# Performance work log

Hardware: AMD Instinct MI355X
Metric: run time of the kernel (lower is better)

The kernel has to match this reference:

```python
import math
import jax, jax.numpy as jnp
import numpy as np

GROUPS = 32
EPS = 1e-5


def group_norm(x, w, b):
    # x: [B, C, H, W]
    B, C, H, W = x.shape
    xg = x.reshape(B, GROUPS, C // GROUPS, H, W)
    mean = xg.mean(axis=(2, 3, 4), keepdims=True)
    var = xg.var(axis=(2, 3, 4), keepdims=True)
    xg = (xg - mean) * jax.lax.rsqrt(var + EPS)
    x = xg.reshape(B, C, H, W)
    return x * w[None, :, None, None] + b[None, :, None, None]


def setup_inputs() -> dict:
    key = jax.random.key(0)
    ks = jax.random.split(key, 4)
    B, C, H, W = 16, 512, 32, 32
    x = jax.random.normal(ks[0], (B, C, H, W), dtype=jnp.float32)
    norm_w = jnp.ones((C,), dtype=jnp.float32)
    norm_b = jnp.zeros((C,), dtype=jnp.float32)
    qkv_w = jax.random.normal(ks[1], (3 * C, C), dtype=jnp.float32) / math.sqrt(C)
    qkv_b = jnp.zeros((3 * C,), dtype=jnp.float32)
    proj_w = jax.random.normal(ks[2], (C, C), dtype=jnp.float32) / math.sqrt(C)
    proj_b = jnp.zeros((C,), dtype=jnp.float32)
    return {"x": x, "norm_w": norm_w, "norm_b": norm_b,
            "qkv_w": qkv_w, "qkv_b": qkv_b,
            "proj_w": proj_w, "proj_b": proj_b}


def reference(x, norm_w, norm_b, qkv_w, qkv_b, proj_w, proj_b):
    B, C, H, W = x.shape
    xn = group_norm(x, norm_w, norm_b)
    # 1x1 conv == channel matmul: [B,3C,H,W]
    qkv = jnp.einsum('oc,bchw->bohw', qkv_w, xn) + qkv_b[None, :, None, None]
    q, k, v = jnp.split(qkv, 3, axis=1)
    q = q.reshape(B, C, H * W).transpose(0, 2, 1)  # [B, HW, C]
    k = k.reshape(B, C, H * W)                     # [B, C, HW]
    v = v.reshape(B, C, H * W).transpose(0, 2, 1)  # [B, HW, C]
    attn = jax.nn.softmax(jnp.einsum('bnc,bcm->bnm', q, k) / math.sqrt(C), axis=-1)
    h = jnp.einsum('bnm,bmc->bnc', attn, v)        # [B, HW, C]
    h = h.transpose(0, 2, 1).reshape(B, C, H, W)
    out = jnp.einsum('oc,bchw->bohw', proj_w, h) + proj_b[None, :, None, None]
    return out + x
```

## Files before the change

kernel.cpp:

```cpp
#include <hip/hip_runtime.h>

#define GLD16(gp, lp) __builtin_amdgcn_global_load_lds( \
    (const __attribute__((address_space(1))) void*)(gp), \
    (__attribute__((address_space(3))) void*)(lp), 16, 0, 0)

typedef __attribute__((ext_vector_type(8))) short bf16x8;
typedef __attribute__((ext_vector_type(4))) float f32x4;

__device__ __forceinline__ short f2bf(float f) {
    union { float f; unsigned u; } x; x.f = f;
    unsigned r = x.u + 0x7fffu + ((x.u >> 16) & 1u);
    return (short)(r >> 16);
}
__device__ __forceinline__ float bf2f(short s) {
    union { unsigned u; float f; } x;
    x.u = ((unsigned)(unsigned short)s) << 16;
    return x.f;
}
__device__ __forceinline__ int xcd_swz(int id, int n) {
    return (id & 7) * (n >> 3) + (id >> 3);
}

__global__ __launch_bounds__(256) void prep(
    const float* __restrict__ qkv_w, const float* __restrict__ proj_w,
    short* __restrict__ wq, short* __restrict__ wp,
    const float* __restrict__ x, float* __restrict__ mean, float* __restrict__ rstd)
{
    if (blockIdx.x < 1024) {
        int idx = blockIdx.x * 256 + threadIdx.x;
        const int NQ4 = (1536 * 512) / 4;
        float4 f; short4 s;
        if (idx < NQ4) {
            f = ((const float4*)qkv_w)[idx];
            s.x = f2bf(f.x); s.y = f2bf(f.y); s.z = f2bf(f.z); s.w = f2bf(f.w);
            ((short4*)wq)[idx] = s;
        } else {
            int j = idx - NQ4;
            f = ((const float4*)proj_w)[j];
            s.x = f2bf(f.x); s.y = f2bf(f.y); s.z = f2bf(f.z); s.w = f2bf(f.w);
            ((short4*)wp)[j] = s;
        }
    } else {
        int bg = blockIdx.x - 1024;
        const float4* p = (const float4*)(x + (size_t)bg * 16384);
        float s = 0.f, ss = 0.f;
        for (int i = threadIdx.x; i < 4096; i += 256) {
            float4 v = p[i];
            s  += v.x + v.y + v.z + v.w;
            ss += v.x * v.x + v.y * v.y + v.z * v.z + v.w * v.w;
        }
        #pragma unroll
        for (int o = 32; o > 0; o >>= 1) {
            s  += __shfl_down(s, o);
            ss += __shfl_down(ss, o);
        }
        __shared__ float ls[4], lss[4];
        int wave = threadIdx.x >> 6;
        if ((threadIdx.x & 63) == 0) { ls[wave] = s; lss[wave] = ss; }
        __syncthreads();
        if (threadIdx.x == 0) {
            s  = ls[0] + ls[1] + ls[2] + ls[3];
            ss = lss[0] + lss[1] + lss[2] + lss[3];
            float m = s * (1.f / 16384.f);
            float var = ss * (1.f / 16384.f) - m * m;
            mean[bg] = m;
            rstd[bg] = rsqrtf(var + 1e-5f);
        }
    }
}

__global__ __launch_bounds__(256) void gn_apply_t(
    const float* __restrict__ x, const float* __restrict__ w, const float* __restrict__ bb,
    const float* __restrict__ mean, const float* __restrict__ rstd,
    short* __restrict__ xnT)
{
    __shared__ short tile[64][65];
    int b = blockIdx.z, cblk = blockIdx.y, nblk = blockIdx.x;
    int t = threadIdx.x;
    int nl = t & 63;
    int cb = t >> 6;
    #pragma unroll
    for (int i = 0; i < 16; ++i) {
        int cl = cb * 16 + i;
        int cg = cblk * 64 + cl;
        int bgid = b * 32 + (cg >> 4);
        float sc = rstd[bgid] * w[cg];
        float sh = bb[cg] - mean[bgid] * sc;
        float xv = x[((size_t)(b * 512 + cg)) * 1024 + nblk * 64 + nl];
        tile[cl][nl] = f2bf(xv * sc + sh);
    }
    __syncthreads();
    int ng = t >> 4;
    int c4 = (t & 15) * 4;
    #pragma unroll
    for (int p = 0; p < 4; ++p) {
        int nl2 = p * 16 + ng;
        short4 sv;
        sv.x = tile[c4 + 0][nl2];
        sv.y = tile[c4 + 1][nl2];
        sv.z = tile[c4 + 2][nl2];
        sv.w = tile[c4 + 3][nl2];
        *(short4*)&xnT[((size_t)(b * 1024 + nblk * 64 + nl2)) * 512 + cblk * 64 + c4] = sv;
    }
}

template<int NT>
__device__ __forceinline__ void gemm256_8p(
    const short* __restrict__ A, const short* __restrict__ B,
    const int lda, const int ldb, short* lds, f32x4 acc[8][4])
{
    const int tid  = threadIdx.x;
    const int lane = tid & 63;
    const int wave = tid >> 6;
    const int wm = wave >> 2;
    const int wn = wave & 3;
    const int fr = lane & 15;
    const int fk = lane >> 4;

    const short* pa[2]; const short* pb[2]; int la[2], lb[2];
    #pragma unroll
    for (int i = 0; i < 2; ++i) {
        int cid = i * 512 + tid;
        int row = cid >> 2, sl = cid & 3;
        int csw = sl ^ ((row >> 1) & 3);
        pa[i] = A + (size_t)row * lda + csw * 8;
        pb[i] = B + (size_t)row * ldb + csw * 8;
        la[i] = cid * 8;
        lb[i] = 8192 + cid * 8;
    }

    #pragma unroll
    for (int i = 0; i < 2; ++i) GLD16(pa[i],      lds + la[i]);
    #pragma unroll
    for (int i = 0; i < 2; ++i) GLD16(pb[i],      lds + lb[i]);
    #pragma unroll
    for (int i = 0; i < 2; ++i) GLD16(pa[i] + 32, lds + 16384 + la[i]);
    #pragma unroll
    for (int i = 0; i < 2; ++i) GLD16(pb[i] + 32, lds + 16384 + lb[i]);
    asm volatile("s_waitcnt vmcnt(4)" ::: "memory");
    asm volatile("s_barrier" ::: "memory");

    const int arow0 = wm * 128 + fr;
    const int brow0 = wn * 64 + fr;

    int base = 0, sbase = 32768, kst = 64;
    for (int t = 0; t < NT; ++t) {
        const short* lA = lds + base;
        const short* lB = lds + base + 8192;
        const bool pre = (t + 2 < NT);

        if (pre) {
            GLD16(pa[0] + kst, lds + sbase + la[0]);
            GLD16(pa[1] + kst, lds + sbase + la[1]);
        }
        bf16x8 af[8], bf0[2];
        #pragma unroll
        for (int m = 0; m < 8; ++m) {
            int R = arow0 + m * 16;
            af[m] = *(const bf16x8*)&lA[R * 32 + ((fk ^ ((R >> 1) & 3)) << 3)];
        }
        #pragma unroll
        for (int n = 0; n < 2; ++n) {
            int R = brow0 + n * 16;
            bf0[n] = *(const bf16x8*)&lB[R * 32 + ((fk ^ ((R >> 1) & 3)) << 3)];
        }
        asm volatile("s_barrier" ::: "memory");
        __builtin_amdgcn_s_setprio(1);
        #pragma unroll
        for (int m = 0; m < 8; ++m)
            #pragma unroll
            for (int n = 0; n < 2; ++n)
                acc[m][n] = __builtin_amdgcn_mfma_f32_16x16x32_bf16(af[m], bf0[n], acc[m][n], 0, 0, 0);
        __builtin_amdgcn_s_setprio(0);

        if (pre) {
            GLD16(pb[0] + kst, lds + sbase + lb[0]);
            GLD16(pb[1] + kst, lds + sbase + lb[1]);
        }
        bf16x8 bf1[2];
        #pragma unroll
        for (int n = 0; n < 2; ++n) {
            int R = brow0 + (n + 2) * 16;
            bf1[n] = *(const bf16x8*)&lB[R * 32 + ((fk ^ ((R >> 1) & 3)) << 3)];
        }
        asm volatile("s_barrier" ::: "memory");
        __builtin_amdgcn_s_setprio(1);
        #pragma unroll
        for (int m = 0; m < 8; ++m)
            #pragma unroll
            for (int n = 0; n < 2; ++n)
                acc[m][n + 2] = __builtin_amdgcn_mfma_f32_16x16x32_bf16(af[m], bf1[n], acc[m][n + 2], 0, 0, 0);
        __builtin_amdgcn_s_setprio(0);

        if (pre)                 asm volatile("s_waitcnt vmcnt(4)" ::: "memory");
        else if (t + 1 < NT)     asm volatile("s_waitcnt vmcnt(0)" ::: "memory");
        asm volatile("s_barrier" ::: "memory");
        __builtin_amdgcn_sched_barrier(0);
        base  = (base  == 32768) ? 0 : base  + 16384;
        sbase = (sbase == 32768) ? 0 : sbase + 16384;
        kst += 32;
    }
}

template<int NT>
__device__ __forceinline__ void gemm128x256(
    const short* __restrict__ A, const short* __restrict__ B,
    const int lda, const int ldb, short* lds, f32x4 acc[4][4])
{
    const int tid  = threadIdx.x;
    const int lane = tid & 63;
    const int wave = tid >> 6;
    const int wm = wave >> 2;
    const int wn = wave & 3;
    const int fr = lane & 15;
    const int fk = lane >> 4;

    const short* pa; int la;
    {
        int row = tid >> 2, sl = tid & 3;
        int csw = sl ^ ((row >> 1) & 3);
        pa = A + (size_t)row * lda + csw * 8;
        la = tid * 8;
    }
    const short* pb[2]; int lb[2];
    #pragma unroll
    for (int i = 0; i < 2; ++i) {
        int cid = i * 512 + tid;
        int row = cid >> 2, sl = cid & 3;
        int csw = sl ^ ((row >> 1) & 3);
        pb[i] = B + (size_t)row * ldb + csw * 8;
        lb[i] = 4096 + cid * 8;
    }

    GLD16(pa, lds + la);
    #pragma unroll
    for (int i = 0; i < 2; ++i) GLD16(pb[i], lds + lb[i]);
    GLD16(pa + 32, lds + 12288 + la);
    #pragma unroll
    for (int i = 0; i < 2; ++i) GLD16(pb[i] + 32, lds + 12288 + lb[i]);
    asm volatile("s_waitcnt vmcnt(3)" ::: "memory");
    asm volatile("s_barrier" ::: "memory");

    const int arow0 = wm * 64 + fr;
    const int brow0 = wn * 64 + fr;

    int base = 0, sbase = 24576, kst = 64;
    for (int t = 0; t < NT; ++t) {
        const short* lA = lds + base;
        const short* lB = lds + base + 4096;
        const bool pre = (t + 2 < NT);

        if (pre) GLD16(pa + kst, lds + sbase + la);
        bf16x8 af[4], bf0[2];
        #pragma unroll
        for (int m = 0; m < 4; ++m) {
            int R = arow0 + m * 16;
            af[m] = *(const bf16x8*)&lA[R * 32 + ((fk ^ ((R >> 1) & 3)) << 3)];
        }
        #pragma unroll
        for (int n = 0; n < 2; ++n) {
            int R = brow0 + n * 16;
            bf0[n] = *(const bf16x8*)&lB[R * 32 + ((fk ^ ((R >> 1) & 3)) << 3)];
        }
        asm volatile("s_barrier" ::: "memory");
        __builtin_amdgcn_s_setprio(1);
        #pragma unroll
        for (int m = 0; m < 4; ++m)
            #pragma unroll
            for (int n = 0; n < 2; ++n)
                acc[m][n] = __builtin_amdgcn_mfma_f32_16x16x32_bf16(af[m], bf0[n], acc[m][n], 0, 0, 0);
        __builtin_amdgcn_s_setprio(0);

        if (pre) {
            GLD16(pb[0] + kst, lds + sbase + lb[0]);
            GLD16(pb[1] + kst, lds + sbase + lb[1]);
        }
        bf16x8 bf1[2];
        #pragma unroll
        for (int n = 0; n < 2; ++n) {
            int R = brow0 + (n + 2) * 16;
            bf1[n] = *(const bf16x8*)&lB[R * 32 + ((fk ^ ((R >> 1) & 3)) << 3)];
        }
        asm volatile("s_barrier" ::: "memory");
        __builtin_amdgcn_s_setprio(1);
        #pragma unroll
        for (int m = 0; m < 4; ++m)
            #pragma unroll
            for (int n = 0; n < 2; ++n)
                acc[m][n + 2] = __builtin_amdgcn_mfma_f32_16x16x32_bf16(af[m], bf1[n], acc[m][n + 2], 0, 0, 0);
        __builtin_amdgcn_s_setprio(0);

        if (pre)                 asm volatile("s_waitcnt vmcnt(3)" ::: "memory");
        else if (t + 1 < NT)     asm volatile("s_waitcnt vmcnt(0)" ::: "memory");
        asm volatile("s_barrier" ::: "memory");
        __builtin_amdgcn_sched_barrier(0);
        base  = (base  == 24576) ? 0 : base  + 12288;
        sbase = (sbase == 24576) ? 0 : sbase + 12288;
        kst += 32;
    }
}

#define EPI_IDX8() \
    const int lane = threadIdx.x & 63; \
    const int wave = threadIdx.x >> 6; \
    const int wm = wave >> 2; \
    const int wn = wave & 3; \
    const int fq = lane >> 4; \
    const int fcol = lane & 15;

__global__ __launch_bounds__(512, 2) void qkv_gemm(
    const short* __restrict__ wq, const float* __restrict__ qkv_b,
    const short* __restrict__ xnT,
    short* __restrict__ qT, short* __restrict__ kT, short* __restrict__ vv)
{
    __shared__ short lds[49152];
    int wg = xcd_swz(blockIdx.x, 384);
    const int bm = wg % 6, bn = wg / 6;
    const short* A  = wq + (size_t)bm * 256 * 512;
    const short* Bb = xnT + (size_t)bn * 256 * 512;
    f32x4 acc[8][4];
    #pragma unroll
    for (int m = 0; m < 8; ++m)
        #pragma unroll
        for (int n = 0; n < 4; ++n) acc[m][n] = (f32x4){0.f, 0.f, 0.f, 0.f};
    gemm256_8p<16>(A, Bb, 512, 512, lds, acc);

    EPI_IDX8();
    const int region = bm >> 1;
    const float qscale = 0.04419417382415922f;

    #pragma unroll
    for (int m = 0; m < 8; ++m) {
        int o0 = bm * 256 + wm * 128 + m * 16 + fq * 4;
        float4 bias = *(const float4*)&qkv_b[o0];
        float bb4[4] = {bias.x, bias.y, bias.z, bias.w};
        #pragma unroll
        for (int n = 0; n < 4; ++n) {
            int cf = bn * 256 + wn * 64 + n * 16 + fcol;
            int b = cf >> 10, col = cf & 1023;
            f32x4 a = acc[m][n];
            if (region == 0) {
                short4 sv;
                sv.x = f2bf((a[0] + bb4[0]) * qscale);
                sv.y = f2bf((a[1] + bb4[1]) * qscale);
                sv.z = f2bf((a[2] + bb4[2]) * qscale);
                sv.w = f2bf((a[3] + bb4[3]) * qscale);
                *(short4*)&qT[((size_t)(b * 1024 + col)) * 512 + o0] = sv;
            } else if (region == 1) {
                short4 sv;
                sv.x = f2bf(a[0] + bb4[0]);
                sv.y = f2bf(a[1] + bb4[1]);
                sv.z = f2bf(a[2] + bb4[2]);
                sv.w = f2bf(a[3] + bb4[3]);
                *(short4*)&kT[((size_t)(b * 1024 + col)) * 512 + (o0 - 512)] = sv;
            } else {
                #pragma unroll
                for (int r = 0; r < 4; ++r)
                    vv[((size_t)(b * 512 + (o0 - 1024 + r))) * 1024 + col] = f2bf(a[r] + bb4[r]);
            }
        }
    }
}

__global__ __launch_bounds__(512, 2) void s_gemm(
    const short* __restrict__ kT, const short* __restrict__ qT, short* __restrict__ S)
{
    __shared__ short lds[49152];
    int wg = xcd_swz(blockIdx.x, 256);
    const int bn = wg & 3, bm = (wg >> 2) & 3, b = wg >> 4;
    const short* A  = kT + ((size_t)b * 1024 + bm * 256) * 512;
    const short* Bb = qT + ((size_t)b * 1024 + bn * 256) * 512;
    f32x4 acc[8][4];
    #pragma unroll
    for (int m = 0; m < 8; ++m)
        #pragma unroll
        for (int n = 0; n < 4; ++n) acc[m][n] = (f32x4){0.f, 0.f, 0.f, 0.f};
    gemm256_8p<16>(A, Bb, 512, 512, lds, acc);

    EPI_IDX8();
    #pragma unroll
    for (int m = 0; m < 8; ++m) {
        int m0 = bm * 256 + wm * 128 + m * 16 + fq * 4;
        #pragma unroll
        for (int n = 0; n < 4; ++n) {
            int ncol = bn * 256 + wn * 64 + n * 16 + fcol;
            f32x4 a = acc[m][n];
            short4 sv;
            sv.x = f2bf(a[0]); sv.y = f2bf(a[1]); sv.z = f2bf(a[2]); sv.w = f2bf(a[3]);
            *(short4*)&S[((size_t)(b * 1024 + ncol)) * 1024 + m0] = sv;
        }
    }
}

__global__ __launch_bounds__(256) void softmax_rows(short* __restrict__ S)
{
    const int wave = threadIdx.x >> 6;
    const int lane = threadIdx.x & 63;
    size_t row = (size_t)blockIdx.x * 4 + wave;
    short* p = S + row * 1024;
    short4 raw[4];
    float v[16];
    #pragma unroll
    for (int i = 0; i < 4; ++i) raw[i] = ((short4*)p)[lane + 64 * i];
    #pragma unroll
    for (int i = 0; i < 4; ++i) {
        v[i * 4 + 0] = bf2f(raw[i].x);
        v[i * 4 + 1] = bf2f(raw[i].y);
        v[i * 4 + 2] = bf2f(raw[i].z);
        v[i * 4 + 3] = bf2f(raw[i].w);
    }
    float mx = v[0];
    #pragma unroll
    for (int i = 1; i < 16; ++i) mx = fmaxf(mx, v[i]);
    #pragma unroll
    for (int o = 1; o < 64; o <<= 1) mx = fmaxf(mx, __shfl_xor(mx, o));
    float sum = 0.f;
    #pragma unroll
    for (int i = 0; i < 16; ++i) { v[i] = __expf(v[i] - mx); sum += v[i]; }
    #pragma unroll
    for (int o = 1; o < 64; o <<= 1) sum += __shfl_xor(sum, o);
    float inv = 1.f / sum;
    #pragma unroll
    for (int i = 0; i < 4; ++i) {
        short4 sv;
        sv.x = f2bf(v[i * 4 + 0] * inv);
        sv.y = f2bf(v[i * 4 + 1] * inv);
        sv.z = f2bf(v[i * 4 + 2] * inv);
        sv.w = f2bf(v[i * 4 + 3] * inv);
        ((short4*)p)[lane + 64 * i] = sv;
    }
}

__global__ __launch_bounds__(512, 4) void pv_gemm(
    const short* __restrict__ vv, const short* __restrict__ P, short* __restrict__ h)
{
    __shared__ short lds[36864];
    int wg = xcd_swz(blockIdx.x, 256);
    const int bn = wg & 3, bm = (wg >> 2) & 3, b = wg >> 4;
    const short* A  = vv + ((size_t)b * 512 + bm * 128) * 1024;
    const short* Bb = P + ((size_t)b * 1024 + bn * 256) * 1024;
    f32x4 acc[4][4];
    #pragma unroll
    for (int m = 0; m < 4; ++m)
        #pragma unroll
        for (int n = 0; n < 4; ++n) acc[m][n] = (f32x4){0.f, 0.f, 0.f, 0.f};
    gemm128x256<32>(A, Bb, 1024, 1024, lds, acc);

    EPI_IDX8();
    #pragma unroll
    for (int m = 0; m < 4; ++m) {
        int c0 = bm * 128 + wm * 64 + m * 16 + fq * 4;
        #pragma unroll
        for (int n = 0; n < 4; ++n) {
            int ncol = bn * 256 + wn * 64 + n * 16 + fcol;
            f32x4 a = acc[m][n];
            short4 sv;
            sv.x = f2bf(a[0]); sv.y = f2bf(a[1]); sv.z = f2bf(a[2]); sv.w = f2bf(a[3]);
            *(short4*)&h[((size_t)(b * 1024 + ncol)) * 512 + c0] = sv;
        }
    }
}

__global__ __launch_bounds__(512, 4) void proj_gemm(
    const short* __restrict__ wp, const float* __restrict__ proj_b,
    const short* __restrict__ h, const float* __restrict__ x, float* __restrict__ out)
{
    __shared__ short lds[36864];
    int wg = xcd_swz(blockIdx.x, 256);
    const int bm = wg & 3, bn = wg >> 2;
    const short* A  = wp + (size_t)bm * 128 * 512;
    const short* Bb = h + (size_t)bn * 256 * 512;
    f32x4 acc[4][4];
    #pragma unroll
    for (int m = 0; m < 4; ++m)
        #pragma unroll
        for (int n = 0; n < 4; ++n) acc[m][n] = (f32x4){0.f, 0.f, 0.f, 0.f};
    gemm128x256<16>(A, Bb, 512, 512, lds, acc);

    EPI_IDX8();
    #pragma unroll
    for (int m = 0; m < 4; ++m) {
        int o0 = bm * 128 + wm * 64 + m * 16 + fq * 4;
        float4 pb = *(const float4*)&proj_b[o0];
        float pb4[4] = {pb.x, pb.y, pb.z, pb.w};
        #pragma unroll
        for (int n = 0; n < 4; ++n) {
            int cf = bn * 256 + wn * 64 + n * 16 + fcol;
            int b = cf >> 10, col = cf & 1023;
            f32x4 a = acc[m][n];
            #pragma unroll
            for (int r = 0; r < 4; ++r) {
                size_t idx = ((size_t)(b * 512 + o0 + r)) * 1024 + col;
                out[idx] = a[r] + pb4[r] + x[idx];
            }
        }
    }
}

extern "C" void kernel_launch(void* const* d_in, const int* in_sizes, int n_in,
                              void* d_out, int out_size, void* d_ws, size_t ws_size,
                              hipStream_t stream) {
    const float* x      = (const float*)d_in[0];
    const float* norm_w = (const float*)d_in[1];
    const float* norm_b = (const float*)d_in[2];
    const float* qkv_w  = (const float*)d_in[3];
    const float* qkv_b  = (const float*)d_in[4];
    const float* proj_w = (const float*)d_in[5];
    const float* proj_b = (const float*)d_in[6];
    float* out = (float*)d_out;

    char* ws = (char*)d_ws;
    size_t off = 0;
    auto alloc = [&](size_t bytes) {
        void* p = ws + off;
        off = (off + bytes + 255) & ~(size_t)255;
        return p;
    };
    float* mean = (float*)alloc(512 * 4);
    float* rstd = (float*)alloc(512 * 4);
    short* wq   = (short*)alloc((size_t)1536 * 512 * 2);
    short* wp   = (short*)alloc((size_t)512 * 512 * 2);
    short* xnT  = (short*)alloc((size_t)16 * 1024 * 512 * 2);
    short* qT   = (short*)alloc((size_t)16 * 1024 * 512 * 2);
    short* kT   = (short*)alloc((size_t)16 * 1024 * 512 * 2);
    short* vv   = (short*)alloc((size_t)16 * 512 * 1024 * 2);
    short* S    = (short*)alloc((size_t)16 * 1024 * 1024 * 2);
    short* h    = xnT;

    prep<<<1536, 256, 0, stream>>>(qkv_w, proj_w, wq, wp, x, mean, rstd);
    gn_apply_t<<<dim3(16, 8, 16), 256, 0, stream>>>(x, norm_w, norm_b, mean, rstd, xnT);
    qkv_gemm<<<384, 512, 0, stream>>>(wq, qkv_b, xnT, qT, kT, vv);
    s_gemm<<<256, 512, 0, stream>>>(kT, qT, S);
    softmax_rows<<<4096, 256, 0, stream>>>(S);
    pv_gemm<<<256, 512, 0, stream>>>(vv, S, h);
    proj_gemm<<<256, 512, 0, stream>>>(wp, proj_b, h, x, out);
}
```

Before: 228.3 us.

## Fuse softmax exp into score GEMM epilogue and defer normalization to PV GEMM

Drops the separate softmax kernel. The S GEMM epilogue now writes exp(S), clamped at 30, with no max subtraction, and accumulates per-row sums through atomics into a new rowsum buffer. The PV GEMM scales its output by the reciprocal row sum. This removes a full read and write pass over the bf16 score matrix and one kernel launch. In exchange it relies on scores being small enough that skipping max subtraction stays accurate, adds atomics and a memset, and also lowers launch_bounds occupancy hints on pv and proj.

```diff
diff --git a/kernel.cpp b/kernel.cpp
--- a/kernel.cpp
+++ b/kernel.cpp
@@ -363,7 +363,8 @@
 }
 
 __global__ __launch_bounds__(512, 2) void s_gemm(
-    const short* __restrict__ kT, const short* __restrict__ qT, short* __restrict__ S)
+    const short* __restrict__ kT, const short* __restrict__ qT,
+    short* __restrict__ S, float* __restrict__ rowsum)
 {
     __shared__ short lds[49152];
     int wg = xcd_swz(blockIdx.x, 256);
@@ -378,6 +379,7 @@
     gemm256_8p<16>(A, Bb, 512, 512, lds, acc);
 
     EPI_IDX8();
+    float rs[4] = {0.f, 0.f, 0.f, 0.f};
     #pragma unroll
     for (int m = 0; m < 8; ++m) {
         int m0 = bm * 256 + wm * 128 + m * 16 + fq * 4;
@@ -385,54 +387,31 @@
         for (int n = 0; n < 4; ++n) {
             int ncol = bn * 256 + wn * 64 + n * 16 + fcol;
             f32x4 a = acc[m][n];
+            float e0 = __expf(fminf(a[0], 30.f));
+            float e1 = __expf(fminf(a[1], 30.f));
+            float e2 = __expf(fminf(a[2], 30.f));
+            float e3 = __expf(fminf(a[3], 30.f));
             short4 sv;
-            sv.x = f2bf(a[0]); sv.y = f2bf(a[1]); sv.z = f2bf(a[2]); sv.w = f2bf(a[3]);
+            sv.x = f2bf(e0); sv.y = f2bf(e1); sv.z = f2bf(e2); sv.w = f2bf(e3);
             *(short4*)&S[((size_t)(b * 1024 + ncol)) * 1024 + m0] = sv;
-        }
-    }
-}
-
-__global__ __launch_bounds__(256) void softmax_rows(short* __restrict__ S)
-{
-    const int wave = threadIdx.x >> 6;
-    const int lane = threadIdx.x & 63;
-    size_t row = (size_t)blockIdx.x * 4 + wave;
-    short* p = S + row * 1024;
-    short4 raw[4];
-    float v[16];
-    #pragma unroll
-    for (int i = 0; i < 4; ++i) raw[i] = ((short4*)p)[lane + 64 * i];
-    #pragma unroll
-    for (int i = 0; i < 4; ++i) {
-        v[i * 4 + 0] = bf2f(raw[i].x);
-        v[i * 4 + 1] = bf2f(raw[i].y);
-        v[i * 4 + 2] = bf2f(raw[i].z);
-        v[i * 4 + 3] = bf2f(raw[i].w);
-    }
-    float mx = v[0];
-    #pragma unroll
-    for (int i = 1; i < 16; ++i) mx = fmaxf(mx, v[i]);
-    #pragma unroll
-    for (int o = 1; o < 64; o <<= 1) mx = fmaxf(mx, __shfl_xor(mx, o));
-    float sum = 0.f;
-    #pragma unroll
-    for (int i = 0; i < 16; ++i) { v[i] = __expf(v[i] - mx); sum += v[i]; }
-    #pragma unroll
-    for (int o = 1; o < 64; o <<= 1) sum += __shfl_xor(sum, o);
-    float inv = 1.f / sum;
-    #pragma unroll
-    for (int i = 0; i < 4; ++i) {
-        short4 sv;
-        sv.x = f2bf(v[i * 4 + 0] * inv);
-        sv.y = f2bf(v[i * 4 + 1] * inv);
-        sv.z = f2bf(v[i * 4 + 2] * inv);
-        sv.w = f2bf(v[i * 4 + 3] * inv);
-        ((short4*)p)[lane + 64 * i] = sv;
-    }
-}
-
-__global__ __launch_bounds__(512, 4) void pv_gemm(
-    const short* __restrict__ vv, const short* __restrict__ P, short* __restrict__ h)
+            rs[n] += e0 + e1 + e2 + e3;
+        }
+    }
+    #pragma unroll
+    for (int n = 0; n < 4; ++n) {
+        float v = rs[n];
+        v += __shfl_xor(v, 16);
+        v += __shfl_xor(v, 32);
+        if (lane < 16) {
+            int ncol = bn * 256 + wn * 64 + n * 16 + lane;
+            atomicAdd(&rowsum[b * 1024 + ncol], v);
+        }
+    }
+}
+
+__global__ __launch_bounds__(512, 2) void pv_gemm(
+    const short* __restrict__ vv, const short* __restrict__ P,
+    const float* __restrict__ rowsum, short* __restrict__ h)
 {
     __shared__ short lds[36864];
     int wg = xcd_swz(blockIdx.x, 256);
@@ -447,6 +426,12 @@
     gemm128x256<32>(A, Bb, 1024, 1024, lds, acc);
 
     EPI_IDX8();
+    float inv[4];
+    #pragma unroll
+    for (int n = 0; n < 4; ++n) {
+        int ncol = bn * 256 + wn * 64 + n * 16 + fcol;
+        inv[n] = 1.f / rowsum[b * 1024 + ncol];
+    }
     #pragma unroll
     for (int m = 0; m < 4; ++m) {
         int c0 = bm * 128 + wm * 64 + m * 16 + fq * 4;
@@ -455,13 +440,14 @@
             int ncol = bn * 256 + wn * 64 + n * 16 + fcol;
             f32x4 a = acc[m][n];
             short4 sv;
-            sv.x = f2bf(a[0]); sv.y = f2bf(a[1]); sv.z = f2bf(a[2]); sv.w = f2bf(a[3]);
+            sv.x = f2bf(a[0] * inv[n]); sv.y = f2bf(a[1] * inv[n]);
+            sv.z = f2bf(a[2] * inv[n]); sv.w = f2bf(a[3] * inv[n]);
             *(short4*)&h[((size_t)(b * 1024 + ncol)) * 512 + c0] = sv;
         }
     }
 }
 
-__global__ __launch_bounds__(512, 4) void proj_gemm(
+__global__ __launch_bounds__(512, 2) void proj_gemm(
     const short* __restrict__ wp, const float* __restrict__ proj_b,
     const short* __restrict__ h, const float* __restrict__ x, float* __restrict__ out)
 {
@@ -516,8 +502,9 @@
         off = (off + bytes + 255) & ~(size_t)255;
         return p;
     };
-    float* mean = (float*)alloc(512 * 4);
-    float* rstd = (float*)alloc(512 * 4);
+    float* mean   = (float*)alloc(512 * 4);
+    float* rstd   = (float*)alloc(512 * 4);
+    float* rowsum = (float*)alloc((size_t)16384 * 4);
     short* wq   = (short*)alloc((size_t)1536 * 512 * 2);
     short* wp   = (short*)alloc((size_t)512 * 512 * 2);
     short* xnT  = (short*)alloc((size_t)16 * 1024 * 512 * 2);
@@ -527,11 +514,11 @@
     short* S    = (short*)alloc((size_t)16 * 1024 * 1024 * 2);
     short* h    = xnT;
 
+    hipMemsetAsync(rowsum, 0, (size_t)16384 * 4, stream);
     prep<<<1536, 256, 0, stream>>>(qkv_w, proj_w, wq, wp, x, mean, rstd);
     gn_apply_t<<<dim3(16, 8, 16), 256, 0, stream>>>(x, norm_w, norm_b, mean, rstd, xnT);
     qkv_gemm<<<384, 512, 0, stream>>>(wq, qkv_b, xnT, qT, kT, vv);
-    s_gemm<<<256, 512, 0, stream>>>(kT, qT, S);
-    softmax_rows<<<4096, 256, 0, stream>>>(S);
-    pv_gemm<<<256, 512, 0, stream>>>(vv, S, h);
+    s_gemm<<<256, 512, 0, stream>>>(kT, qT, S, rowsum);
+    pv_gemm<<<256, 512, 0, stream>>>(vv, S, rowsum, h);
     proj_gemm<<<256, 512, 0, stream>>>(wp, proj_b, h, x, out);
 }
```

Result: faster. 214.2 us (-6.2%).
